# Performance work log

Measured on AMD Instinct MI355X. Metric: run time of the kernel, lower is better.

The kernel has to match this reference:

```python
import jax, jax.numpy as jnp
import numpy as np

NUM_HEADS = 8
STRIDE = 1
PAD = 1


def _conv(x, w, stride=STRIDE, pad=PAD):
    return jax.lax.conv_general_dilated(
        x, w, (stride, stride), [(pad, pad), (pad, pad)],
        dimension_numbers=("NCHW", "OIHW", "NCHW"))


def setup_inputs() -> dict:
    key = jax.random.key(0)
    ks = jax.random.split(key, 5)
    B, C, H, W = 8, 64, 56, 56
    nh = NUM_HEADS
    x = jax.random.normal(ks[0], (B, C, H, W), dtype=jnp.float32)
    # Conv weights, small init for numerical stability
    Wq = jax.random.normal(ks[1], (C * nh, C, 3, 3), dtype=jnp.float32) * 0.05
    Wk = jax.random.normal(ks[2], (C * nh, C, 3, 3), dtype=jnp.float32) * 0.05
    Wv = jax.random.normal(ks[3], (C * nh, C, 3, 3), dtype=jnp.float32) * 0.05
    Wu = jax.random.normal(ks[4], (C, C * nh, 1, 1), dtype=jnp.float32) * 0.05
    return {"x": x, "Wq": Wq, "Wk": Wk, "Wv": Wv, "Wu": Wu}


def reference(x, Wq, Wk, Wv, Wu):
    B, C, H, W = x.shape
    nh = NUM_HEADS
    # projections: [B, nh*C, H, W] -> [B, nh, C, H, W] -> [B, C, nh, H, W]
    def proj(w):
        y = _conv(x, w).reshape(B, nh, C, H, W)
        return jnp.transpose(y, (0, 2, 1, 3, 4))
    q = proj(Wq)  # [B, C, nh, H, W]
    k = proj(Wk)
    v = proj(Wv)
    scale = 1.0 / np.sqrt(C * nh).astype(np.float32)
    # contract over heads axis ('n'), attend over channel axis: [B, Cq, H, W, Ck]
    scores = jnp.einsum("bqnhw,bknhw->bqhwk", q, k) * scale
    attn = jax.nn.softmax(scores, axis=-1)
    # attended: [B, Cq, nh, H, W]
    attended = jnp.einsum("bqhwk,bknhw->bqnhw", attn, v)
    out = _conv(attended.reshape(B, C * nh, H, W), Wu, stride=1, pad=0)
    return jax.nn.relu(out)
```

## Files before the change

### kernel.cpp

```cpp
#include <hip/hip_runtime.h>
#include <hip/hip_bf16.h>

#define HW   56
#define CIN  64
#define OC   512
#define NPIX (HW * HW)
#define PEL  ((size_t)8 * NPIX * OC)

typedef unsigned short ushort_t;
typedef __attribute__((ext_vector_type(8))) short short8;
typedef __attribute__((ext_vector_type(4))) float floatx4;
typedef __attribute__((ext_vector_type(16))) float floatx16;

static __device__ __forceinline__ ushort_t f2bf(float f) {
  __hip_bfloat16 h = __float2bfloat16(f);
  return *(ushort_t*)&h;
}

#if __has_builtin(__builtin_amdgcn_exp2f)
#define EXP2F(x) __builtin_amdgcn_exp2f(x)
#else
#define EXP2F(x) exp2f(x)
#endif

__global__ __launch_bounds__(256)
void prep_kernel(const float* __restrict__ x, const float* __restrict__ W0,
                 const float* __restrict__ W1, const float* __restrict__ W2,
                 const float* __restrict__ Wu, ushort_t* __restrict__ xT,
                 ushort_t* __restrict__ Wb, ushort_t* __restrict__ WuP) {
  __shared__ ushort_t lx[CIN * HW];
  const int bid = blockIdx.x;
  const int tid = threadIdx.x;

  if (bid < 448) {
    const int h = bid % HW, b = bid / HW;
    for (int idx = tid; idx < CIN * HW; idx += 256) {
      int c = idx / HW, w = idx - c * HW;
      lx[idx] = f2bf(x[((size_t)(b * CIN + c) * HW + h) * HW + w]);
    }
    __syncthreads();
    ushort_t* dst = xT + ((size_t)(b * HW + h)) * HW * CIN;
    for (int i = tid; i < (CIN * HW) / 4; i += 256) {
      int e0 = i * 4;
      int w = e0 >> 6, c0 = e0 & 63;
      ushort4 o;
      o.x = lx[(c0 + 0) * HW + w];
      o.y = lx[(c0 + 1) * HW + w];
      o.z = lx[(c0 + 2) * HW + w];
      o.w = lx[(c0 + 3) * HW + w];
      ((ushort4*)dst)[i] = o;
    }
  } else if (bid < 832) {
    const int u = bid - 448;
    const int sel = u / 128;
    const int j = (u % 128) * 4 + (tid >> 6);
    const int cin = tid & 63;
    const float* W = sel == 0 ? W0 : (sel == 1 ? W1 : W2);
    ushort_t* Ds = Wb + (size_t)sel * 9 * OC * CIN;
    const int src = (sel < 2) ? ((j & 7) * 64 + (j >> 3)) : j;
    #pragma unroll
    for (int tap = 0; tap < 9; ++tap)
      Ds[((size_t)tap * OC + j) * CIN + cin] = f2bf(W[(size_t)src * 576 + cin * 9 + tap]);
  } else {
    const int el = (bid - 832) * 256 + tid;
    WuP[el] = f2bf(Wu[el]);
  }
}

#define XLS 72
#define XROW (58 * XLS)

__global__ __launch_bounds__(256, 2)
void conv3x3_qkv(const ushort_t* __restrict__ xT, const ushort_t* __restrict__ Wb,
                 ushort_t* __restrict__ yq) {
  __shared__ __align__(16) ushort_t xl[6 * XROW];

  const int tid  = threadIdx.x;
  const int lane = tid & 63;
  const int wv   = tid >> 6;
  const int g    = blockIdx.x;
  const int ob   = blockIdx.y;
  const int z    = blockIdx.z;
  const int b    = z & 7;
  const int s    = z >> 3;
  const int h0   = g * 4;
  const int l31  = lane & 31;
  const int khi  = lane >> 5;

  const int th    = wv >> 1;
  const int oh    = wv & 1;
  const int tbase = th * 4;

  int rowcol[4], rowv[4];
  #pragma unroll
  for (int t = 0; t < 4; ++t) {
    int p = (tbase + t) * 32 + l31;
    int row = p / HW, ww = p - row * HW;
    rowcol[t] = (row * 58 + ww) * XLS;
    rowv[t] = row;
  }

  const ushort_t* wb0 = Wb + (size_t)s * 9 * OC * CIN +
                        ((size_t)(ob * 128 + oh * 64 + l31)) * CIN + khi * 8;

  for (int r = 0; r < 6; ++r) {
    int gh = h0 - 1 + r;
    const int sw = 2 * ((-r) & 3);
    if (gh >= 0 && gh < HW) {
      const uint4* src = (const uint4*)(xT + ((size_t)(b * HW + gh) * HW) * CIN);
      for (int idx = tid; idx < 448; idx += 256) {
        int w = idx >> 3, c8 = idx & 7;
        int col = 1 + w;
        int p8 = (c8 + sw) & 7;
        *(uint4*)&xl[(r * 58 + col) * XLS + p8 * 8] = src[idx];
      }
      if (tid < 16) {
        int col = (tid >> 3) ? 57 : 0, c8 = tid & 7;
        int p8 = (c8 + sw) & 7;
        *(uint4*)&xl[(r * 58 + col) * XLS + p8 * 8] = (uint4){0, 0, 0, 0};
      }
    } else {
      for (int idx = tid; idx < 464; idx += 256) {
        int col = idx >> 3, c8 = idx & 7;
        int p8 = (c8 + sw) & 7;
        *(uint4*)&xl[(r * 58 + col) * XLS + p8 * 8] = (uint4){0, 0, 0, 0};
      }
    }
  }

  short8 Bc0 = *(const short8*)(wb0);
  short8 Bc1 = *(const short8*)(wb0 + 32 * CIN);

  floatx16 acc[4][2];
  #pragma unroll
  for (int t = 0; t < 4; ++t) {
    acc[t][0] = (floatx16)(0.0f);
    acc[t][1] = (floatx16)(0.0f);
  }

  __syncthreads();

  #pragma unroll
  for (int step = 0; step < 36; ++step) {
    const int tap = step >> 2, ck = step & 3;
    short8 Bn0, Bn1;
    if (step < 35) {
      const int ntap = (step + 1) >> 2, nck = (step + 1) & 3;
      const size_t boff = (size_t)ntap * (OC * CIN) + nck * 16;
      Bn0 = *(const short8*)(wb0 + boff);
      Bn1 = *(const short8*)(wb0 + boff + 32 * CIN);
    } else {
      Bn0 = Bc0; Bn1 = Bc1;
    }
    const int kh = tap / 3, kw = tap - kh * 3;
    #pragma unroll
    for (int t = 0; t < 4; ++t) {
      if (tbase + t < 7) {
        int chunk = (khi + 2 * ((-(rowv[t] + kh)) & 3) + 2 * ck) & 7;
        short8 af = *(const short8*)&xl[rowcol[t] + (kh * 58 + kw) * XLS + chunk * 8];
        acc[t][0] = __builtin_amdgcn_mfma_f32_32x32x16_bf16(af, Bc0, acc[t][0], 0, 0, 0);
        acc[t][1] = __builtin_amdgcn_mfma_f32_32x32x16_bf16(af, Bc1, acc[t][1], 0, 0, 0);
      }
    }
    Bc0 = Bn0; Bc1 = Bn1;
  }

  ushort_t* y = yq + (size_t)s * PEL;
  const int ocb = ob * 128 + oh * 64 + l31;
  #pragma unroll
  for (int t = 0; t < 4; ++t) {
    if (tbase + t < 7) {
      #pragma unroll
      for (int i = 0; i < 16; ++i) {
        int p = (tbase + t) * 32 + (i & 3) + 8 * (i >> 2) + 4 * khi;
        int row = p / HW, ww = p - row * HW;
        size_t pb = ((size_t)((b * HW + h0 + row) * HW + ww)) * OC;
        y[pb + ocb]      = f2bf(acc[t][0][i]);
        y[pb + ocb + 32] = f2bf(acc[t][1][i]);
      }
    }
  }
}

#define PST  72
#define A2ST 520

__global__ __launch_bounds__(256, 3)
void attn_kernel(const ushort_t* __restrict__ q, const ushort_t* __restrict__ k,
                 const ushort_t* __restrict__ v, const ushort_t* __restrict__ WuP,
                 float* __restrict__ out) {
  __shared__ __align__(16) ushort_t Pl[4][64 * PST];
  __shared__ __align__(16) ushort_t a2[16 * A2ST];

  const int tid  = threadIdx.x;
  const int lane = tid & 63;
  const int wv   = tid >> 6;
  const int l15  = lane & 15;
  const int quad = lane >> 4;
  const int p0   = blockIdx.x * 16;
  const int b    = blockIdx.y;
  const size_t ibase = ((size_t)b * NPIX + p0) * 512;

  ushort_t* Pw = &Pl[wv][0];
  const float scale2 = 0.063758723f;

  auto loadpix = [&](int plocal, short8 qf[4], short8 kf[4], short8 vf[2]) {
    const ushort_t* qp = q + ibase + (size_t)plocal * 512;
    const ushort_t* kp = k + ibase + (size_t)plocal * 512;
    const ushort_t* vp = v + ibase + (size_t)plocal * 512;
    #pragma unroll
    for (int nt = 0; nt < 4; ++nt)
      qf[nt] = *(const short8*)(qp + (nt * 16 + l15) * 8);
    #pragma unroll
    for (int mt = 0; mt < 4; ++mt) {
      kf[mt] = (short8){0, 0, 0, 0, 0, 0, 0, 0};
      if (quad == 0) kf[mt] = *(const short8*)(kp + (mt * 16 + l15) * 8);
    }
    #pragma unroll
    for (int ck = 0; ck < 2; ++ck)
      vf[ck] = *(const short8*)(vp + (l15 & 7) * 64 + ck * 32 + quad * 8);
  };

  short8 qf[4], kf[4], vf[2];
  loadpix(wv * 4, qf, kf, vf);

  #pragma unroll
  for (int i = 0; i < 4; ++i) {
    const int plocal = wv * 4 + i;
    short8 qn[4], kn[4], vn[2];
    if (i < 3) loadpix(plocal + 1, qn, kn, vn);

    floatx4 S[4][4];
    #pragma unroll
    for (int mt = 0; mt < 4; ++mt)
      #pragma unroll
      for (int nt = 0; nt < 4; ++nt) S[mt][nt] = (floatx4){0.f, 0.f, 0.f, 0.f};
    #pragma unroll
    for (int mt = 0; mt < 4; ++mt)
      #pragma unroll
      for (int nt = 0; nt < 4; ++nt)
        S[mt][nt] = __builtin_amdgcn_mfma_f32_16x16x32_bf16(kf[mt], qf[nt], S[mt][nt], 0, 0, 0);

    float inv[4];
    #pragma unroll
    for (int nt = 0; nt < 4; ++nt) {
      float e[4][4];
      #pragma unroll
      for (int mt = 0; mt < 4; ++mt)
        #pragma unroll
        for (int r = 0; r < 4; ++r)
          e[mt][r] = EXP2F(S[mt][nt][r] * scale2);
      float sm[4];
      #pragma unroll
      for (int mt = 0; mt < 4; ++mt)
        sm[mt] = (e[mt][0] + e[mt][1]) + (e[mt][2] + e[mt][3]);
      float sum = (sm[0] + sm[1]) + (sm[2] + sm[3]);
      sum += __shfl_xor(sum, 16);
      sum += __shfl_xor(sum, 32);
      inv[nt] = __builtin_amdgcn_rcpf(sum);
      #pragma unroll
      for (int mt = 0; mt < 4; ++mt) {
        ushort4 w4;
        w4.x = f2bf(e[mt][0]);
        w4.y = f2bf(e[mt][1]);
        w4.z = f2bf(e[mt][2]);
        w4.w = f2bf(e[mt][3]);
        *(ushort4*)&Pw[(nt * 16 + l15) * PST + mt * 16 + quad * 4] = w4;
      }
    }

    floatx4 T[4];
    #pragma unroll
    for (int nt = 0; nt < 4; ++nt) T[nt] = (floatx4){0.f, 0.f, 0.f, 0.f};
    #pragma unroll
    for (int ck = 0; ck < 2; ++ck) {
      #pragma unroll
      for (int nt = 0; nt < 4; ++nt) {
        short8 pf = *(const short8*)&Pw[(nt * 16 + l15) * PST + ck * 32 + quad * 8];
        T[nt] = __builtin_amdgcn_mfma_f32_16x16x32_bf16(vf[ck], pf, T[nt], 0, 0, 0);
      }
    }
    if (quad < 2) {
      #pragma unroll
      for (int nt = 0; nt < 4; ++nt) {
        ushort4 w4;
        w4.x = f2bf(T[nt][0] * inv[nt]);
        w4.y = f2bf(T[nt][1] * inv[nt]);
        w4.z = f2bf(T[nt][2] * inv[nt]);
        w4.w = f2bf(T[nt][3] * inv[nt]);
        *(ushort4*)&a2[plocal * A2ST + (nt * 16 + l15) * 8 + quad * 4] = w4;
      }
    }

    if (i < 3) {
      #pragma unroll
      for (int z = 0; z < 4; ++z) { qf[z] = qn[z]; kf[z] = kn[z]; }
      vf[0] = vn[0];
      vf[1] = vn[1];
    }
  }
  __syncthreads();

  floatx4 O = (floatx4){0.f, 0.f, 0.f, 0.f};
  #pragma unroll
  for (int ck = 0; ck < 16; ++ck) {
    short8 aw = *(const short8*)(WuP + (size_t)(wv * 16 + l15) * 512 + ck * 32 + quad * 8);
    short8 bw = *(const short8*)&a2[l15 * A2ST + ck * 32 + quad * 8];
    O = __builtin_amdgcn_mfma_f32_16x16x32_bf16(aw, bw, O, 0, 0, 0);
  }
  #pragma unroll
  for (int r = 0; r < 4; ++r) {
    int co = wv * 16 + quad * 4 + r;
    out[((size_t)b * 64 + co) * NPIX + p0 + l15] = fmaxf(O[r], 0.f);
  }
}

extern "C" void kernel_launch(void* const* d_in, const int* in_sizes, int n_in,
                              void* d_out, int out_size, void* d_ws, size_t ws_size,
                              hipStream_t stream) {
  const float* x  = (const float*)d_in[0];
  const float* Wq = (const float*)d_in[1];
  const float* Wk = (const float*)d_in[2];
  const float* Wv = (const float*)d_in[3];
  const float* Wu = (const float*)d_in[4];
  float* out = (float*)d_out;

  const size_t xT_elems = (size_t)8 * NPIX * CIN;
  const size_t w_elems  = (size_t)9 * OC * CIN;
  const size_t wu_elems = (size_t)64 * 512;
  ushort_t* xT  = (ushort_t*)d_ws;
  ushort_t* Wb  = xT + xT_elems;
  ushort_t* WuP = Wb + 3 * w_elems;
  ushort_t* q   = WuP + wu_elems;
  ushort_t* k   = q + PEL;
  ushort_t* v   = k + PEL;

  prep_kernel<<<960, 256, 0, stream>>>(x, Wq, Wk, Wv, Wu, xT, Wb, WuP);

  dim3 cgrid(14, 4, 24);
  conv3x3_qkv<<<cgrid, 256, 0, stream>>>(xT, Wb, q);

  attn_kernel<<<dim3(NPIX / 16, 8), 256, 0, stream>>>(q, k, v, WuP, out);
}
```

Baseline: 177.2 us.

## Compute Q, K and V projections in one block, reusing the staged input tile

The conv kernel now loops over the three projections (q, k, v) inside each block instead of launching a separate block per projection. The padded input halo is staged into LDS once and reused for all three, which cuts global loads and LDS fills by a factor of three. The weight prefetch now loads a whole tap's fragments (8 short8 per thread) one tap ahead rather than one k-chunk ahead. In exchange the grid shrinks from 1344 to 448 blocks, leaving less parallelism on a large GPU, and more registers are live from the wider weight prefetch.

```diff
diff --git a/kernel.cpp b/kernel.cpp
--- a/kernel.cpp
+++ b/kernel.cpp
@@ -80,9 +80,7 @@
   const int wv   = tid >> 6;
   const int g    = blockIdx.x;
   const int ob   = blockIdx.y;
-  const int z    = blockIdx.z;
-  const int b    = z & 7;
-  const int s    = z >> 3;
+  const int b    = blockIdx.z;
   const int h0   = g * 4;
   const int l31  = lane & 31;
   const int khi  = lane >> 5;
@@ -100,8 +98,7 @@
     rowv[t] = row;
   }
 
-  const ushort_t* wb0 = Wb + (size_t)s * 9 * OC * CIN +
-                        ((size_t)(ob * 128 + oh * 64 + l31)) * CIN + khi * 8;
+  const ushort_t* wb0 = Wb + ((size_t)(ob * 128 + oh * 64 + l31)) * CIN + khi * 8;
 
   for (int r = 0; r < 6; ++r) {
     int gh = h0 - 1 + r;
@@ -128,55 +125,67 @@
     }
   }
 
-  short8 Bc0 = *(const short8*)(wb0);
-  short8 Bc1 = *(const short8*)(wb0 + 32 * CIN);
-
-  floatx16 acc[4][2];
-  #pragma unroll
-  for (int t = 0; t < 4; ++t) {
-    acc[t][0] = (floatx16)(0.0f);
-    acc[t][1] = (floatx16)(0.0f);
-  }
+  short8 BfA[2][4], BfB[2][4];
+  #pragma unroll
+  for (int gq = 0; gq < 2; ++gq)
+    #pragma unroll
+    for (int ck = 0; ck < 4; ++ck)
+      BfA[gq][ck] = *(const short8*)(wb0 + gq * (32 * CIN) + ck * 16);
 
   __syncthreads();
 
-  #pragma unroll
-  for (int step = 0; step < 36; ++step) {
-    const int tap = step >> 2, ck = step & 3;
-    short8 Bn0, Bn1;
-    if (step < 35) {
-      const int ntap = (step + 1) >> 2, nck = (step + 1) & 3;
-      const size_t boff = (size_t)ntap * (OC * CIN) + nck * 16;
-      Bn0 = *(const short8*)(wb0 + boff);
-      Bn1 = *(const short8*)(wb0 + boff + 32 * CIN);
-    } else {
-      Bn0 = Bc0; Bn1 = Bc1;
-    }
-    const int kh = tap / 3, kw = tap - kh * 3;
+  #pragma unroll 1
+  for (int s = 0; s < 3; ++s) {
+    floatx16 acc[4][2];
+    #pragma unroll
+    for (int t = 0; t < 4; ++t) {
+      acc[t][0] = (floatx16)(0.0f);
+      acc[t][1] = (floatx16)(0.0f);
+    }
+
+    #pragma unroll
+    for (int tap = 0; tap < 9; ++tap) {
+      const int wtap = s * 9 + tap;
+      if (wtap < 26) {
+        #pragma unroll
+        for (int gq = 0; gq < 2; ++gq)
+          #pragma unroll
+          for (int ck = 0; ck < 4; ++ck)
+            BfB[gq][ck] = *(const short8*)(wb0 + (size_t)(wtap + 1) * (OC * CIN) +
+                                           gq * (32 * CIN) + ck * 16);
+      }
+      const int kh = tap / 3, kw = tap - kh * 3;
+      #pragma unroll
+      for (int ck = 0; ck < 4; ++ck) {
+        #pragma unroll
+        for (int t = 0; t < 4; ++t) {
+          if (tbase + t < 7) {
+            int chunk = (khi + 2 * ((-(rowv[t] + kh)) & 3) + 2 * ck) & 7;
+            short8 af = *(const short8*)&xl[rowcol[t] + (kh * 58 + kw) * XLS + chunk * 8];
+            acc[t][0] = __builtin_amdgcn_mfma_f32_32x32x16_bf16(af, BfA[0][ck], acc[t][0], 0, 0, 0);
+            acc[t][1] = __builtin_amdgcn_mfma_f32_32x32x16_bf16(af, BfA[1][ck], acc[t][1], 0, 0, 0);
+          }
+        }
+      }
+      #pragma unroll
+      for (int gq = 0; gq < 2; ++gq)
+        #pragma unroll
+        for (int ck = 0; ck < 4; ++ck) BfA[gq][ck] = BfB[gq][ck];
+    }
+
+    ushort_t* y = yq + (size_t)s * PEL;
+    const int ocb = ob * 128 + oh * 64 + l31;
     #pragma unroll
     for (int t = 0; t < 4; ++t) {
       if (tbase + t < 7) {
-        int chunk = (khi + 2 * ((-(rowv[t] + kh)) & 3) + 2 * ck) & 7;
-        short8 af = *(const short8*)&xl[rowcol[t] + (kh * 58 + kw) * XLS + chunk * 8];
-        acc[t][0] = __builtin_amdgcn_mfma_f32_32x32x16_bf16(af, Bc0, acc[t][0], 0, 0, 0);
-        acc[t][1] = __builtin_amdgcn_mfma_f32_32x32x16_bf16(af, Bc1, acc[t][1], 0, 0, 0);
-      }
-    }
-    Bc0 = Bn0; Bc1 = Bn1;
-  }
-
-  ushort_t* y = yq + (size_t)s * PEL;
-  const int ocb = ob * 128 + oh * 64 + l31;
-  #pragma unroll
-  for (int t = 0; t < 4; ++t) {
-    if (tbase + t < 7) {
-      #pragma unroll
-      for (int i = 0; i < 16; ++i) {
-        int p = (tbase + t) * 32 + (i & 3) + 8 * (i >> 2) + 4 * khi;
-        int row = p / HW, ww = p - row * HW;
-        size_t pb = ((size_t)((b * HW + h0 + row) * HW + ww)) * OC;
-        y[pb + ocb]      = f2bf(acc[t][0][i]);
-        y[pb + ocb + 32] = f2bf(acc[t][1][i]);
+        #pragma unroll
+        for (int i = 0; i < 16; ++i) {
+          int p = (tbase + t) * 32 + (i & 3) + 8 * (i >> 2) + 4 * khi;
+          int row = p / HW, ww = p - row * HW;
+          size_t pb = ((size_t)((b * HW + h0 + row) * HW + ww)) * OC;
+          y[pb + ocb]      = f2bf(acc[t][0][i]);
+          y[pb + ocb + 32] = f2bf(acc[t][1][i]);
+        }
       }
     }
   }
@@ -337,7 +346,7 @@
 
   prep_kernel<<<960, 256, 0, stream>>>(x, Wq, Wk, Wv, Wu, xT, Wb, WuP);
 
-  dim3 cgrid(14, 4, 24);
+  dim3 cgrid(14, 4, 8);
   conv3x3_qkv<<<cgrid, 256, 0, stream>>>(xT, Wb, q);
 
   attn_kernel<<<dim3(NPIX / 16, 8), 256, 0, stream>>>(q, k, v, WuP, out);
```

Result: slower. 230.8 us (+30.2%).
